# Performance work log

Hardware: AMD Instinct MI355X
Metric: run time of the kernel (lower is better)

## Reference

```python
import jax, jax.numpy as jnp
import numpy as np

N, E = 50000, 1600000
D_IN, D_OUT = 256, 64
ALPHA = 0.2        # LeakyReLU slope used on attention logits (self.leakyrelu)
BT_SLOPE = 0.01    # F.leaky_relu default slope inside relu_bt


def _xavier_normal(key, shape, gain):
    fan_in, fan_out = shape[0], shape[1]
    std = gain * np.sqrt(2.0 / (fan_in + fan_out))
    return jax.random.normal(key, shape, dtype=jnp.float32) * std


def relu_bt(x):
    # -threshold(-leaky_relu(x), -t, -t) == min(leaky_relu(x), t), t = ||x||_inf (detached)
    t = jax.lax.stop_gradient(jnp.max(jnp.abs(x)))
    y = jnp.where(x >= 0, x, BT_SLOPE * x)
    return jnp.minimum(y, t)


def setup_inputs() -> dict:
    key = jax.random.key(0)
    k0, k1, k2, k3, k4, k5 = jax.random.split(key, 6)
    inp = jax.random.normal(k0, (N, D_IN), dtype=jnp.float32)
    edge = jax.random.randint(k1, (2, E), 0, N, dtype=jnp.int64)
    W_high = _xavier_normal(k2, (D_IN, D_OUT), 1.414)
    W_low = _xavier_normal(k3, (D_IN, D_OUT), 1.414)
    a_high = _xavier_normal(k4, (1, D_OUT), 1.414)
    a_low = _xavier_normal(k5, (1, D_OUT), 1.414)
    return {"input": inp, "edge": edge, "W_high": W_high, "W_low": W_low,
            "a_high": a_high, "a_low": a_low}


def reference(input, edge, W_high, W_low, a_high, a_low):
    n = input.shape[0]
    src, dst = edge[0], edge[1]

    h_high = relu_bt(input @ W_high)  # [N, D_OUT]
    h_low = relu_bt(input @ W_low)    # [N, D_OUT]

    # a @ (h[src] -/+ h[dst])^T == (a.h)[src] -/+ (a.h)[dst]: compute per-node scalar
    # projections first, then gather scalars per edge (avoids [E, D_OUT] edge features).
    s_high = h_high @ a_high[0]       # [N]
    s_low = h_low @ a_low[0]          # [N]

    def lrelu(x):
        return jnp.where(x >= 0, x, ALPHA * x)

    edge_e_high = jnp.exp(-lrelu(s_high[src] - s_high[dst]))  # [E]
    edge_e_low = jnp.exp(-lrelu(s_low[src] + s_low[dst]))     # [E]
    # dropout p=0.0 -> identity

    # sparse A @ ones -> per-row sum of attention weights
    rowsum_high = jax.ops.segment_sum(edge_e_high, src, num_segments=n)[:, None]
    rowsum_low = jax.ops.segment_sum(edge_e_low, src, num_segments=n)[:, None]

    # sparse A @ h -> weighted aggregation of neighbor features
    hp_high = jax.ops.segment_sum(edge_e_high[:, None] * h_high[dst], src, num_segments=n)
    hp_low = jax.ops.segment_sum(edge_e_low[:, None] * h_low[dst], src, num_segments=n)

    hp_high = hp_high / (rowsum_high + 1e-16)
    hp_low = hp_low / (rowsum_low + 1e-16)

    # concat=True branch
    return relu_bt(jnp.concatenate([hp_high, hp_low], axis=1))  # [N, 2*D_OUT]
```

## Files before the change

kernel.cpp:

```cpp
#include <hip/hip_runtime.h>
#include <hip/hip_bf16.h>
#include <cstdint>

#define NN    50000
#define NE    1600000
#define DIN   256
#define DOUT  64
#define CAPS  96
#define CAPD  95

#define BKT   196
#define BCAP  10240
#define EPB   4096
#define EPT   16
#define NBIN  391
#define MTB   32
#define NGEMM 1563

typedef __attribute__((ext_vector_type(8))) short frag8;
typedef __attribute__((ext_vector_type(4))) float fragc;

union PK { __hip_bfloat162 b2; uint32_t u; };
union CH { frag8 v; uint32_t u[4]; };

__device__ __forceinline__ float leaky01(float x) { return x >= 0.f ? x : 0.01f * x; }

__device__ __forceinline__ uint32_t pk2(float lo, float hi) {
  PK p; p.b2 = __float22bfloat162_rn(make_float2(lo, hi)); return p.u;
}

__device__ __forceinline__ int   bcast_i(int v, int lane) {
  return __builtin_amdgcn_readlane(v, lane);
}

__device__ __forceinline__ float bfH(uint32_t u) { return __uint_as_float(u << 16); }
__device__ __forceinline__ float bfL(uint32_t u) { return __uint_as_float(u & 0xffff0000u); }

__global__ __launch_bounds__(256) void prep_kernel(
    const float* __restrict__ Wh, const float* __restrict__ Wl,
    __hip_bfloat16* __restrict__ Wt, int* __restrict__ cursor)
{
  if (blockIdx.x == 0 && threadIdx.x < BKT) cursor[threadIdx.x] = 0;
  int g = blockIdx.x * 256 + threadIdx.x;
  if (g < 2 * DOUT * DIN) {
    int m = g >> 14, rem = g & 16383;
    int n = rem >> 8, k = rem & 255;
    float v = (m ? Wl : Wh)[k * DOUT + n];
    Wt[g] = __float2bfloat16(v);
  }
}

__global__ __launch_bounds__(256) void fused_kernel(
    const float* __restrict__ inp, const __hip_bfloat16* __restrict__ Wt,
    const float* __restrict__ ah, const float* __restrict__ al,
    const int* __restrict__ edge, int* __restrict__ cursor,
    uint32_t* __restrict__ binned, uint32_t* __restrict__ HL,
    float2* __restrict__ ss)
{
  __shared__ __align__(16) char smem[20480];

  const int idx = blockIdx.x;
  const int t = threadIdx.x;

  if (idx < NBIN) {
    uint32_t* stage  = (uint32_t*)smem;
    int*      hist   = (int*)(smem + 16384);
    int*      cur    = (int*)(smem + 17408);
    int*      base_g = (int*)(smem + 18192);
    int*      scan_s = (int*)(smem + 18976);

    const int e0 = idx * EPB;
    uint32_t v[EPT];
#pragma unroll
    for (int i = 0; i < EPT; i++) {
      int e = e0 + i * 256 + t;
      if (e < NE) {
        uint32_t s = (uint32_t)edge[e];
        uint32_t d = (uint32_t)edge[NE + e];
        v[i] = (s << 16) | d;
      } else {
        v[i] = 0xFFFFFFFFu;
      }
    }
    if (t < 256) hist[t] = 0;
    for (int b = t; b < BKT; b += 256) cur[b] = 0;
    __syncthreads();
#pragma unroll
    for (int i = 0; i < EPT; i++) {
      int b = v[i] >> 24;
      if (b < BKT) atomicAdd(&hist[b], 1);
    }
    __syncthreads();
    if (t < 64) {
      int carry = 0;
#pragma unroll
      for (int seg = 0; seg < 4; seg++) {
        int i = seg * 64 + t;
        int h = hist[i];
        int s = h;
#pragma unroll
        for (int off = 1; off < 64; off <<= 1) {
          int o = __shfl_up(s, off);
          if (t >= off) s += o;
        }
        int excl = carry + s - h;
        if (i <= BKT) scan_s[i] = excl;
        carry += bcast_i(s, 63);
      }
    }
    __syncthreads();
    for (int b = t; b < BKT; b += 256) {
      int h = hist[b];
      base_g[b] = h ? atomicAdd(&cursor[b], h) : 0;
    }
    __syncthreads();
#pragma unroll
    for (int i = 0; i < EPT; i++) {
      int b = v[i] >> 24;
      if (b < BKT) {
        int pos = atomicAdd(&cur[b], 1);
        stage[scan_s[b] + pos] = v[i];
      }
    }
    __syncthreads();
    const int total = scan_s[BKT];
    for (int i = t; i < total; i += 256) {
      uint32_t sv = stage[i];
      int bb = sv >> 24;
      int ofs = base_g[bb] + (i - scan_s[bb]);
      if (ofs < BCAP) binned[(size_t)bb * BCAP + ofs] = sv;
    }
    return;
  }

  const int gid = idx - NBIN;
  const int n0 = gid * MTB;
  const int lane = t & 63;
  const int w = t >> 6;
  const int quad = lane >> 4, nn = lane & 15;

  const frag8* Wt8 = (const frag8*)Wt;
  const int bbase = ((w * 16 + nn) << 5) + quad;
  frag8 bH[8], bL[8];
#pragma unroll
  for (int q = 0; q < 8; q++) {
    bH[q] = Wt8[bbase + (q << 2)];
    bL[q] = Wt8[2048 + bbase + (q << 2)];
  }

  const float4* inp4 = (const float4*)inp;
  const int l5 = t & 31;
  const int rw = t >> 5;
  {
    const int q8 = l5 >> 2, qd = l5 & 3;
#pragma unroll
    for (int i = 0; i < 4; i++) {
      int row = i * 8 + rw;
      int node = n0 + row;
      float4 a0 = make_float4(0.f, 0.f, 0.f, 0.f), a1 = a0;
      if (node < NN) {
        a0 = inp4[(size_t)node * 64 + l5 * 2];
        a1 = inp4[(size_t)node * 64 + l5 * 2 + 1];
      }
      int c = ((row >> 4) << 9) | (q8 << 6) | (qd << 4) | (row & 15);
      int B = c << 4;
      B ^= ((B >> 8) & 7) << 4;
      CH ch;
      ch.u[0] = pk2(a0.x, a0.y);
      ch.u[1] = pk2(a0.z, a0.w);
      ch.u[2] = pk2(a1.x, a1.y);
      ch.u[3] = pk2(a1.z, a1.w);
      *(frag8*)(smem + B) = ch.v;
    }
  }
  __syncthreads();

  fragc accH[2], accL[2];
#pragma unroll
  for (int m = 0; m < 2; m++) {
    accH[m] = (fragc){0.f, 0.f, 0.f, 0.f};
    accL[m] = (fragc){0.f, 0.f, 0.f, 0.f};
  }

#pragma unroll
  for (int q = 0; q < 8; q++) {
#pragma unroll
    for (int mt = 0; mt < 2; mt++) {
      int R = (mt << 13) + (q << 10) + (lane << 4);
      R ^= ((R >> 8) & 7) << 4;
      frag8 af = *(const frag8*)(smem + R);
      accH[mt] = __builtin_amdgcn_mfma_f32_16x16x32_bf16(af, bH[q], accH[mt], 0, 0, 0);
      accL[mt] = __builtin_amdgcn_mfma_f32_16x16x32_bf16(af, bL[q], accL[mt], 0, 0, 0);
    }
  }
  __syncthreads();

  float* sred = (float*)smem;
  const float ahv = ah[w * 16 + nn];
  const float alv = al[w * 16 + nn];
#pragma unroll
  for (int mt = 0; mt < 2; mt++) {
#pragma unroll
    for (int r = 0; r < 4; r++) {
      int rowb = (mt << 4) + (quad << 2) + r;
      int node = n0 + rowb;
      float hH = leaky01(accH[mt][r]);
      float hL = leaky01(accL[mt][r]);
      if (node < NN) HL[(size_t)node * DOUT + w * 16 + nn] = pk2(hH, hL);
      float pH = hH * ahv, pL = hL * alv;
#pragma unroll
      for (int off = 1; off < 16; off <<= 1) {
        pH += __shfl_xor(pH, off);
        pL += __shfl_xor(pL, off);
      }
      if (nn == 0) {
        sred[rowb * 8 + w]     = pH;
        sred[rowb * 8 + 4 + w] = pL;
      }
    }
  }
  __syncthreads();
  if (t < 32) {
    int node = n0 + t;
    if (node < NN) {
      float sH = sred[t * 8 + 0] + sred[t * 8 + 1] + sred[t * 8 + 2] + sred[t * 8 + 3];
      float sL = sred[t * 8 + 4] + sred[t * 8 + 5] + sred[t * 8 + 6] + sred[t * 8 + 7];
      ss[node] = make_float2(sH, sL);
    }
  }
}

__global__ __launch_bounds__(256) void csr_kernel(
    const uint32_t* __restrict__ binned, const int* __restrict__ cursor,
    unsigned short* __restrict__ col)
{
  __shared__ __align__(16) unsigned short lst[64][CAPS];
  __shared__ int cnt[64];
  const int blk = blockIdx.x;
  const int b    = ((blk >> 5) << 3) + (blk & 7);
  const int part = (blk >> 3) & 3;
  if (b >= BKT) return;
  const int t = threadIdx.x;
  if (t < 64) cnt[t] = 0;
  __syncthreads();
  int n = cursor[b]; if (n > BCAP) n = BCAP;
  const uint32_t* eb = binned + (size_t)b * BCAP;
  for (int i = t; i < n; i += 256) {
    uint32_t v = eb[i];
    int src = v >> 16, dst = v & 0xffff;
    int loc = src & 255;
    if ((loc >> 6) == part) {
      int pos = atomicAdd(&cnt[loc & 63], 1);
      if (pos < CAPD) lst[loc & 63][1 + pos] = (unsigned short)dst;
    }
  }
  __syncthreads();
  if (t < 64) {
    int c = cnt[t]; if (c > CAPD) c = CAPD;
    lst[t][0] = (unsigned short)c;
  }
  __syncthreads();
  const int base_node = (b << 8) + (part << 6);
  int4* dst4 = (int4*)(col + (size_t)base_node * CAPS);
  const int4* src4 = (const int4*)&lst[0][0];
  for (int i = t; i < 64 * CAPS / 8; i += 256) {
    int node = base_node + i / (CAPS / 8);
    if (node < NN) dst4[i] = src4[i];
  }
}

__global__ __launch_bounds__(256) void agg_kernel(
    const uint32_t* __restrict__ HL, const float2* __restrict__ ss,
    const unsigned short* __restrict__ col, float* __restrict__ out)
{
  int wave = (blockIdx.x * blockDim.x + threadIdx.x) >> 6;
  int lane = threadIdx.x & 63;
  if (wave >= NN) return;
  const int n = wave;
  const unsigned short* cl = col + (size_t)n * CAPS;
  int d = cl[0]; if (d > CAPD) d = CAPD;

  const float2 sn = ss[n];
  const uint2* HL2 = (const uint2*)HL;

  const int vodd4 = (lane & 32) >> 3;
  const int lo31  = lane & 31;

  float accH0 = 0.f, accH1 = 0.f, accL0 = 0.f, accL1 = 0.f;
  float rsH = 0.f, rsL = 0.f;

  for (int base = 0; base < d; base += 64) {
    int m = d - base; if (m > 64) m = 64;
    int   dst_l = 0;
    float eh_l = 0.f, el_l = 0.f;
    if (lane < m) {
      dst_l = cl[1 + base + lane];
      float2 sd = ss[dst_l];
      float xh = sn.x - sd.x;
      xh = (xh >= 0.f) ? xh : 0.2f * xh;
      eh_l = __expf(-xh);
      float xl = sn.y + sd.y;
      xl = (xl >= 0.f) ? xl : 0.2f * xl;
      el_l = __expf(-xl);
    }
    const int ehb = __float_as_int(eh_l);
    const int elb = __float_as_int(el_l);
    const int pj = (m + 1) >> 1;
    for (int jj = 0; jj < pj; jj += 4) {
      int vdd[4]; float veh[4], vel[4]; uint2 u[4];
#pragma unroll
      for (int x = 0; x < 4; x++) {
        int ib = vodd4 + ((jj + x) << 3);
        vdd[x] = __builtin_amdgcn_ds_bpermute(ib, dst_l);
        veh[x] = __int_as_float(__builtin_amdgcn_ds_bpermute(ib, ehb));
        vel[x] = __int_as_float(__builtin_amdgcn_ds_bpermute(ib, elb));
      }
#pragma unroll
      for (int x = 0; x < 4; x++)
        u[x] = HL2[(((uint32_t)vdd[x]) << 5) + lo31];
#pragma unroll
      for (int x = 0; x < 4; x++) {
        accH0 += veh[x] * bfH(u[x].x);
        accL0 += vel[x] * bfL(u[x].x);
        accH1 += veh[x] * bfH(u[x].y);
        accL1 += vel[x] * bfL(u[x].y);
      }
    }
    float rh = eh_l, rl = el_l;
#pragma unroll
    for (int off = 1; off < 64; off <<= 1) {
      rh += __shfl_xor(rh, off);
      rl += __shfl_xor(rl, off);
    }
    rsH += rh; rsL += rl;
  }

  accH0 += __shfl_xor(accH0, 32);
  accH1 += __shfl_xor(accH1, 32);
  accL0 += __shfl_xor(accL0, 32);
  accL1 += __shfl_xor(accL1, 32);

  float r  = (lane < 32) ? rsH : rsL;
  float a0 = (lane < 32) ? accH0 : accL0;
  float a1 = (lane < 32) ? accH1 : accL1;
  float inv = 1.f / (r + 1e-16f);
  float o0 = leaky01(a0 * inv);
  float o1 = leaky01(a1 * inv);
  float2* op = (float2*)(out + (size_t)n * 128 + ((lane & 32) << 1) + (lo31 << 1));
  *op = make_float2(o0, o1);
}

extern "C" void kernel_launch(void* const* d_in, const int* in_sizes, int n_in,
                              void* d_out, int out_size, void* d_ws, size_t ws_size,
                              hipStream_t stream) {
  const float* inp  = (const float*)d_in[0];
  const int*   edge = (const int*)d_in[1];
  const float* Wh   = (const float*)d_in[2];
  const float* Wl   = (const float*)d_in[3];
  const float* ah   = (const float*)d_in[4];
  const float* al   = (const float*)d_in[5];
  float* out = (float*)d_out;

  char* ws = (char*)d_ws;
  uint32_t* HL     = (uint32_t*)(ws + 0);
  float2*   ss     = (float2*)  (ws + 12800000);
  unsigned short* col = (unsigned short*)(ws + 13200000);
  uint32_t* binned = (uint32_t*)(ws + 32400000);
  int*      cursor = (int*)     (ws + 40428160);
  __hip_bfloat16* Wt = (__hip_bfloat16*)(ws + 13200000);

  prep_kernel<<<128, 256, 0, stream>>>(Wh, Wl, Wt, cursor);
  fused_kernel<<<NBIN + NGEMM, 256, 0, stream>>>(inp, Wt, ah, al, edge,
                                                 cursor, binned, HL, ss);
  csr_kernel<<<800, 256, 0, stream>>>(binned, cursor, col);
  agg_kernel<<<NN / 4, 256, 0, stream>>>(HL, ss, col, out);
}
```

Before: 191.3 us.

## Split GEMM blocks across binning and CSR kernels to overlap phases

The node-feature GEMM is split into two parts. The first 650 tiles run alongside edge binning in the first fused kernel, and the remaining tiles run alongside CSR construction in a second fused kernel that replaces the standalone csr_kernel. This hides the latency-bound CSR pass behind GEMM work and removes a lightly loaded launch. Wt moves to its own workspace region so that CSR writes to col no longer overlap it while the GEMM is still reading it. The 650/913 split ratio is a tuning choice that may unbalance the two kernels.

```diff
diff --git a/kernel.cpp b/kernel.cpp
--- a/kernel.cpp
+++ b/kernel.cpp
@@ -16,6 +16,8 @@
 #define NBIN  391
 #define MTB   32
 #define NGEMM 1563
+#define NCSR  800
+#define GSPL  650
 
 typedef __attribute__((ext_vector_type(8))) short frag8;
 typedef __attribute__((ext_vector_type(4))) float fragc;
@@ -50,90 +52,11 @@
   }
 }
 
-__global__ __launch_bounds__(256) void fused_kernel(
-    const float* __restrict__ inp, const __hip_bfloat16* __restrict__ Wt,
+__device__ __forceinline__ void gemm_role(
+    int gid, const float* __restrict__ inp, const __hip_bfloat16* __restrict__ Wt,
     const float* __restrict__ ah, const float* __restrict__ al,
-    const int* __restrict__ edge, int* __restrict__ cursor,
-    uint32_t* __restrict__ binned, uint32_t* __restrict__ HL,
-    float2* __restrict__ ss)
-{
-  __shared__ __align__(16) char smem[20480];
-
-  const int idx = blockIdx.x;
-  const int t = threadIdx.x;
-
-  if (idx < NBIN) {
-    uint32_t* stage  = (uint32_t*)smem;
-    int*      hist   = (int*)(smem + 16384);
-    int*      cur    = (int*)(smem + 17408);
-    int*      base_g = (int*)(smem + 18192);
-    int*      scan_s = (int*)(smem + 18976);
-
-    const int e0 = idx * EPB;
-    uint32_t v[EPT];
-#pragma unroll
-    for (int i = 0; i < EPT; i++) {
-      int e = e0 + i * 256 + t;
-      if (e < NE) {
-        uint32_t s = (uint32_t)edge[e];
-        uint32_t d = (uint32_t)edge[NE + e];
-        v[i] = (s << 16) | d;
-      } else {
-        v[i] = 0xFFFFFFFFu;
-      }
-    }
-    if (t < 256) hist[t] = 0;
-    for (int b = t; b < BKT; b += 256) cur[b] = 0;
-    __syncthreads();
-#pragma unroll
-    for (int i = 0; i < EPT; i++) {
-      int b = v[i] >> 24;
-      if (b < BKT) atomicAdd(&hist[b], 1);
-    }
-    __syncthreads();
-    if (t < 64) {
-      int carry = 0;
-#pragma unroll
-      for (int seg = 0; seg < 4; seg++) {
-        int i = seg * 64 + t;
-        int h = hist[i];
-        int s = h;
-#pragma unroll
-        for (int off = 1; off < 64; off <<= 1) {
-          int o = __shfl_up(s, off);
-          if (t >= off) s += o;
-        }
-        int excl = carry + s - h;
-        if (i <= BKT) scan_s[i] = excl;
-        carry += bcast_i(s, 63);
-      }
-    }
-    __syncthreads();
-    for (int b = t; b < BKT; b += 256) {
-      int h = hist[b];
-      base_g[b] = h ? atomicAdd(&cursor[b], h) : 0;
-    }
-    __syncthreads();
-#pragma unroll
-    for (int i = 0; i < EPT; i++) {
-      int b = v[i] >> 24;
-      if (b < BKT) {
-        int pos = atomicAdd(&cur[b], 1);
-        stage[scan_s[b] + pos] = v[i];
-      }
-    }
-    __syncthreads();
-    const int total = scan_s[BKT];
-    for (int i = t; i < total; i += 256) {
-      uint32_t sv = stage[i];
-      int bb = sv >> 24;
-      int ofs = base_g[bb] + (i - scan_s[bb]);
-      if (ofs < BCAP) binned[(size_t)bb * BCAP + ofs] = sv;
-    }
-    return;
-  }
-
-  const int gid = idx - NBIN;
+    uint32_t* __restrict__ HL, float2* __restrict__ ss, char* smem, int t)
+{
   const int n0 = gid * MTB;
   const int lane = t & 63;
   const int w = t >> 6;
@@ -230,43 +153,140 @@
   }
 }
 
-__global__ __launch_bounds__(256) void csr_kernel(
+__global__ __launch_bounds__(256) void fused1_kernel(
+    const float* __restrict__ inp, const __hip_bfloat16* __restrict__ Wt,
+    const float* __restrict__ ah, const float* __restrict__ al,
+    const int* __restrict__ edge, int* __restrict__ cursor,
+    uint32_t* __restrict__ binned, uint32_t* __restrict__ HL,
+    float2* __restrict__ ss)
+{
+  __shared__ __align__(16) char smem[20480];
+
+  const int idx = blockIdx.x;
+  const int t = threadIdx.x;
+
+  if (idx < NBIN) {
+    uint32_t* stage  = (uint32_t*)smem;
+    int*      hist   = (int*)(smem + 16384);
+    int*      cur    = (int*)(smem + 17408);
+    int*      base_g = (int*)(smem + 18192);
+    int*      scan_s = (int*)(smem + 18976);
+
+    const int e0 = idx * EPB;
+    uint32_t v[EPT];
+#pragma unroll
+    for (int i = 0; i < EPT; i++) {
+      int e = e0 + i * 256 + t;
+      if (e < NE) {
+        uint32_t s = (uint32_t)edge[e];
+        uint32_t d = (uint32_t)edge[NE + e];
+        v[i] = (s << 16) | d;
+      } else {
+        v[i] = 0xFFFFFFFFu;
+      }
+    }
+    hist[t] = 0;
+    for (int b = t; b < BKT; b += 256) cur[b] = 0;
+    __syncthreads();
+#pragma unroll
+    for (int i = 0; i < EPT; i++) {
+      int b = v[i] >> 24;
+      if (b < BKT) atomicAdd(&hist[b], 1);
+    }
+    __syncthreads();
+    if (t < 64) {
+      int carry = 0;
+#pragma unroll
+      for (int seg = 0; seg < 4; seg++) {
+        int i = seg * 64 + t;
+        int h = hist[i];
+        int s = h;
+#pragma unroll
+        for (int off = 1; off < 64; off <<= 1) {
+          int o = __shfl_up(s, off);
+          if (t >= off) s += o;
+        }
+        int excl = carry + s - h;
+        if (i <= BKT) scan_s[i] = excl;
+        carry += bcast_i(s, 63);
+      }
+    }
+    __syncthreads();
+    for (int b = t; b < BKT; b += 256) {
+      int h = hist[b];
+      base_g[b] = h ? atomicAdd(&cursor[b], h) : 0;
+    }
+    __syncthreads();
+#pragma unroll
+    for (int i = 0; i < EPT; i++) {
+      int b = v[i] >> 24;
+      if (b < BKT) {
+        int pos = atomicAdd(&cur[b], 1);
+        stage[scan_s[b] + pos] = v[i];
+      }
+    }
+    __syncthreads();
+    const int total = scan_s[BKT];
+    for (int i = t; i < total; i += 256) {
+      uint32_t sv = stage[i];
+      int bb = sv >> 24;
+      int ofs = base_g[bb] + (i - scan_s[bb]);
+      if (ofs < BCAP) binned[(size_t)bb * BCAP + ofs] = sv;
+    }
+    return;
+  }
+
+  gemm_role(idx - NBIN, inp, Wt, ah, al, HL, ss, smem, t);
+}
+
+__global__ __launch_bounds__(256) void fused2_kernel(
+    const float* __restrict__ inp, const __hip_bfloat16* __restrict__ Wt,
+    const float* __restrict__ ah, const float* __restrict__ al,
     const uint32_t* __restrict__ binned, const int* __restrict__ cursor,
-    unsigned short* __restrict__ col)
-{
-  __shared__ __align__(16) unsigned short lst[64][CAPS];
-  __shared__ int cnt[64];
-  const int blk = blockIdx.x;
-  const int b    = ((blk >> 5) << 3) + (blk & 7);
-  const int part = (blk >> 3) & 3;
-  if (b >= BKT) return;
+    unsigned short* __restrict__ col, uint32_t* __restrict__ HL,
+    float2* __restrict__ ss)
+{
+  __shared__ __align__(16) char smem[16640];
+
+  const int idx = blockIdx.x;
   const int t = threadIdx.x;
-  if (t < 64) cnt[t] = 0;
-  __syncthreads();
-  int n = cursor[b]; if (n > BCAP) n = BCAP;
-  const uint32_t* eb = binned + (size_t)b * BCAP;
-  for (int i = t; i < n; i += 256) {
-    uint32_t v = eb[i];
-    int src = v >> 16, dst = v & 0xffff;
-    int loc = src & 255;
-    if ((loc >> 6) == part) {
-      int pos = atomicAdd(&cnt[loc & 63], 1);
-      if (pos < CAPD) lst[loc & 63][1 + pos] = (unsigned short)dst;
-    }
-  }
-  __syncthreads();
-  if (t < 64) {
-    int c = cnt[t]; if (c > CAPD) c = CAPD;
-    lst[t][0] = (unsigned short)c;
-  }
-  __syncthreads();
-  const int base_node = (b << 8) + (part << 6);
-  int4* dst4 = (int4*)(col + (size_t)base_node * CAPS);
-  const int4* src4 = (const int4*)&lst[0][0];
-  for (int i = t; i < 64 * CAPS / 8; i += 256) {
-    int node = base_node + i / (CAPS / 8);
-    if (node < NN) dst4[i] = src4[i];
-  }
+
+  if (idx < NCSR) {
+    unsigned short (*lst)[CAPS] = (unsigned short (*)[CAPS])smem;
+    int* cnt = (int*)(smem + 12288);
+    const int b    = ((idx >> 5) << 3) + (idx & 7);
+    const int part = (idx >> 3) & 3;
+    if (b >= BKT) return;
+    if (t < 64) cnt[t] = 0;
+    __syncthreads();
+    int n = cursor[b]; if (n > BCAP) n = BCAP;
+    const uint32_t* eb = binned + (size_t)b * BCAP;
+    for (int i = t; i < n; i += 256) {
+      uint32_t v = eb[i];
+      int src = v >> 16, dst = v & 0xffff;
+      int loc = src & 255;
+      if ((loc >> 6) == part) {
+        int pos = atomicAdd(&cnt[loc & 63], 1);
+        if (pos < CAPD) lst[loc & 63][1 + pos] = (unsigned short)dst;
+      }
+    }
+    __syncthreads();
+    if (t < 64) {
+      int c = cnt[t]; if (c > CAPD) c = CAPD;
+      lst[t][0] = (unsigned short)c;
+    }
+    __syncthreads();
+    const int base_node = (b << 8) + (part << 6);
+    int4* dst4 = (int4*)(col + (size_t)base_node * CAPS);
+    const int4* src4 = (const int4*)&lst[0][0];
+    for (int i = t; i < 64 * CAPS / 8; i += 256) {
+      int node = base_node + i / (CAPS / 8);
+      if (node < NN) dst4[i] = src4[i];
+    }
+    return;
+  }
+
+  gemm_role(GSPL + idx - NCSR, inp, Wt, ah, al, HL, ss, smem, t);
 }
 
 __global__ __launch_bounds__(256) void agg_kernel(
@@ -365,13 +385,14 @@
   uint32_t* HL     = (uint32_t*)(ws + 0);
   float2*   ss     = (float2*)  (ws + 12800000);
   unsigned short* col = (unsigned short*)(ws + 13200000);
+  __hip_bfloat16* Wt  = (__hip_bfloat16*)(ws + 24000000);
   uint32_t* binned = (uint32_t*)(ws + 32400000);
   int*      cursor = (int*)     (ws + 40428160);
-  __hip_bfloat16* Wt = (__hip_bfloat16*)(ws + 13200000);
 
   prep_kernel<<<128, 256, 0, stream>>>(Wh, Wl, Wt, cursor);
-  fused_kernel<<<NBIN + NGEMM, 256, 0, stream>>>(inp, Wt, ah, al, edge,
+  fused1_kernel<<<NBIN + GSPL, 256, 0, stream>>>(inp, Wt, ah, al, edge,
                                                  cursor, binned, HL, ss);
-  csr_kernel<<<800, 256, 0, stream>>>(binned, cursor, col);
+  fused2_kernel<<<NCSR + (NGEMM - GSPL), 256, 0, stream>>>(inp, Wt, ah, al,
+                                                 binned, cursor, col, HL, ss);
   agg_kernel<<<NN / 4, 256, 0, stream>>>(HL, ss, col, out);
 }
```

Result: no change. 194.9 us (+1.9%).
